# Kernel tuning notes

Hardware: AMD Instinct MI355X
Metric: run time of the kernel (lower is better)

The kernel has to match this reference:

```python
import jax, jax.numpy as jnp
import numpy as np

D_IN = 1024
D_OUT = 1024
N = 4096


def setup_inputs() -> dict:
    key = jax.random.key(0)
    kx, kq, kk, kv = jax.random.split(key, 4)
    x = jax.random.normal(kx, (N, D_IN), dtype=jnp.float32)
    # weights stored as [d_in, d_out] so that x @ W == torch Linear(x)
    s = 1.0 / np.sqrt(D_IN)
    W_q = jax.random.uniform(kq, (D_IN, D_OUT), jnp.float32, -s, s)
    W_k = jax.random.uniform(kk, (D_IN, D_OUT), jnp.float32, -s, s)
    W_v = jax.random.uniform(kv, (D_IN, D_OUT), jnp.float32, -s, s)
    return {"x": x, "W_q": W_q, "W_k": W_k, "W_v": W_v}


def reference(x, W_q, W_k, W_v):
    # x: [N, d_in]; projections -> [N, d_out]
    q = x @ W_q
    k = x @ W_k
    v = x @ W_v
    scale = 1.0 / jnp.sqrt(jnp.asarray(k.shape[-1], dtype=q.dtype))
    scores = (q @ k.T) * scale            # [N, N]
    weights = jax.nn.softmax(scores, axis=-1)
    return weights @ v                     # [N, d_out]
```

## Files before the change

### kernel.cpp

```cpp
#include <hip/hip_runtime.h>
#include <math.h>

typedef _Float16 f16;
typedef __attribute__((ext_vector_type(8))) _Float16 f16x8;
typedef __attribute__((ext_vector_type(4))) _Float16 f16x4;
typedef __attribute__((ext_vector_type(4))) float f32x4;

#define NSEQ 4096
#define DIN 1024
#define DOUT 1024

__device__ __forceinline__ void load16(const void* g, void* l) {
    __builtin_amdgcn_global_load_lds(
        (const __attribute__((address_space(1))) unsigned int*)g,
        (__attribute__((address_space(3))) unsigned int*)l, 16, 0, 0);
}

template <typename OutT>
__global__ __launch_bounds__(256, 2)
void gemm_bt(const f16* __restrict__ A, const f16* __restrict__ B,
             OutT* __restrict__ C, int M, int N, int K,
             int lda, int ldb, int ldc, float scale,
             long bStrideZ, long cStrideZ)
{
    B += (long)blockIdx.z * bStrideZ;
    C += (long)blockIdx.z * cStrideZ;
    __shared__ f16 As[2 * 128 * 32];
    __shared__ f16 Bs[2 * 128 * 32];

    int gx = gridDim.x;
    int bid = blockIdx.y * gx + blockIdx.x;
    int xcd = bid & 7, s = bid >> 3;
    int px = s & 7, rest = s >> 3;
    int py = rest & 3, chunk = rest >> 2;
    int pg = xcd + (chunk << 3);
    int pcols = gx >> 3;
    int lp = 31 - __clz(pcols);
    int bx = ((pg & (pcols - 1)) << 3) + px;
    int by = ((pg >> lp) << 2) + py;

    const int t    = threadIdx.x;
    const int lane = t & 63;
    const int wave = t >> 6;
    const int wm   = (wave >> 1) * 64;
    const int wn   = (wave & 1) * 64;
    const int tile_m = by * 128;
    const int tile_n = bx * 128;
    const int quad = lane >> 4;
    const int l16  = lane & 15;
    const int srow = t >> 2;
    const int scol = (t & 3) * 8;

    f32x4 acc[4][4];
#pragma unroll
    for (int i = 0; i < 4; i++)
#pragma unroll
        for (int j = 0; j < 4; j++)
            acc[i][j] = (f32x4){0.f, 0.f, 0.f, 0.f};

    const f16* Ab = A + (long)(tile_m + srow) * lda + scol;
    const f16* Bb = B + (long)(tile_n + srow) * ldb + scol;
    f16* Asd = As + t * 8;
    f16* Bsd = Bs + t * 8;

    for (int k0 = 0; k0 < K; k0 += 64) {
        load16(Ab + k0, Asd);
        load16(Ab + (long)64 * lda + k0, Asd + 2048);
        load16(Ab + k0 + 32, Asd + 4096);
        load16(Ab + (long)64 * lda + k0 + 32, Asd + 4096 + 2048);
        load16(Bb + k0, Bsd);
        load16(Bb + (long)64 * ldb + k0, Bsd + 2048);
        load16(Bb + k0 + 32, Bsd + 4096);
        load16(Bb + (long)64 * ldb + k0 + 32, Bsd + 4096 + 2048);
        __syncthreads();
#pragma unroll
        for (int p = 0; p < 2; p++) {
            f16x8 a[4], b[4];
#pragma unroll
            for (int i = 0; i < 4; i++)
                a[i] = *(const f16x8*)(As + p * 4096 + (wm + i * 16 + l16) * 32 + quad * 8);
#pragma unroll
            for (int j = 0; j < 4; j++)
                b[j] = *(const f16x8*)(Bs + p * 4096 + (wn + j * 16 + l16) * 32 + quad * 8);
#pragma unroll
            for (int i = 0; i < 4; i++)
#pragma unroll
                for (int j = 0; j < 4; j++)
                    acc[i][j] = __builtin_amdgcn_mfma_f32_16x16x32_f16(
                        a[i], b[j], acc[i][j], 0, 0, 0);
        }
        __syncthreads();
    }
#pragma unroll
    for (int i = 0; i < 4; i++)
#pragma unroll
        for (int j = 0; j < 4; j++)
#pragma unroll
            for (int r = 0; r < 4; r++) {
                int row = tile_m + wm + i * 16 + quad * 4 + r;
                int col = tile_n + wn + j * 16 + l16;
                C[(long)row * ldc + col] = (OutT)(acc[i][j][r] * scale);
            }
}

__global__ void cvt_f16(const float* __restrict__ x, f16* __restrict__ y) {
    int i = (blockIdx.x * 256 + threadIdx.x) * 4;
    f32x4 v = *(const f32x4*)(x + i);
    f16x4 o;
    o.x = (f16)v.x; o.y = (f16)v.y; o.z = (f16)v.z; o.w = (f16)v.w;
    *(f16x4*)(y + i) = o;
}

__global__ void transpose_w3(const float* __restrict__ W0, const float* __restrict__ W1,
                             const float* __restrict__ W2, f16* __restrict__ Wt) {
    __shared__ f16 tile[64][65];
    const float* W = blockIdx.z == 0 ? W0 : (blockIdx.z == 1 ? W1 : W2);
    f16* O = Wt + (long)blockIdx.z * DIN * DOUT;
    int r0 = blockIdx.y * 64;
    int c0 = blockIdx.x * 64;
    int tx = threadIdx.x & 63, ty = threadIdx.x >> 6;
#pragma unroll
    for (int i = 0; i < 16; i++)
        tile[ty + i * 4][tx] = (f16)W[(long)(r0 + ty + i * 4) * DOUT + c0 + tx];
    __syncthreads();
#pragma unroll
    for (int i = 0; i < 16; i++)
        O[(long)(c0 + ty + i * 4) * DIN + r0 + tx] = tile[tx][ty + i * 4];
}

__global__ void transpose_v(const f16* __restrict__ V, f16* __restrict__ Vt) {
    __shared__ f16 tile[64][65];
    int r0 = blockIdx.y * 64;
    int c0 = blockIdx.x * 64;
    int tx = threadIdx.x & 63, ty = threadIdx.x >> 6;
#pragma unroll
    for (int i = 0; i < 16; i++)
        tile[ty + i * 4][tx] = V[(long)(r0 + ty + i * 4) * DOUT + c0 + tx];
    __syncthreads();
#pragma unroll
    for (int i = 0; i < 16; i++)
        Vt[(long)(c0 + ty + i * 4) * NSEQ + r0 + tx] = tile[tx][ty + i * 4];
}

__global__ __launch_bounds__(256)
void softmax_f16(f16* __restrict__ S) {
    const int t = threadIdx.x;
    f16* row = S + (long)blockIdx.x * NSEQ;
    float v[16];
    f16x8 x0 = *(const f16x8*)(row + t * 8);
    f16x8 x1 = *(const f16x8*)(row + 2048 + t * 8);
#pragma unroll
    for (int i = 0; i < 8; i++) { v[i] = (float)x0[i]; v[8 + i] = (float)x1[i]; }
    int lane = t & 63, wave = t >> 6;
    float m = -1e30f;
#pragma unroll
    for (int i = 0; i < 16; i++) m = fmaxf(m, v[i]);
#pragma unroll
    for (int off = 32; off; off >>= 1) m = fmaxf(m, __shfl_xor(m, off, 64));
    __shared__ float redm[4];
    if (lane == 0) redm[wave] = m;
    __syncthreads();
    m = fmaxf(fmaxf(redm[0], redm[1]), fmaxf(redm[2], redm[3]));
    float sum = 0.f;
#pragma unroll
    for (int i = 0; i < 16; i++) { v[i] = __expf(v[i] - m); sum += v[i]; }
#pragma unroll
    for (int off = 32; off; off >>= 1) sum += __shfl_xor(sum, off, 64);
    __shared__ float reds[4];
    if (lane == 0) reds[wave] = sum;
    __syncthreads();
    sum = reds[0] + reds[1] + reds[2] + reds[3];
    float inv = 1.f / sum;
    f16x8 o0, o1;
#pragma unroll
    for (int i = 0; i < 8; i++) {
        o0[i] = (f16)(v[i] * inv);
        o1[i] = (f16)(v[8 + i] * inv);
    }
    *(f16x8*)(row + t * 8) = o0;
    *(f16x8*)(row + 2048 + t * 8) = o1;
}

extern "C" void kernel_launch(void* const* d_in, const int* in_sizes, int n_in,
                              void* d_out, int out_size, void* d_ws, size_t ws_size,
                              hipStream_t stream) {
    const float* x  = (const float*)d_in[0];
    const float* Wq = (const float*)d_in[1];
    const float* Wk = (const float*)d_in[2];
    const float* Wv = (const float*)d_in[3];
    float* out = (float*)d_out;
    char* ws = (char*)d_ws;
    const size_t MB = 1ull << 20;
    f16* xb = (f16*)(ws);
    f16* Wt = (f16*)(ws + 8 * MB);
    f16* Qb = (f16*)(ws + 14 * MB);
    f16* Kb = (f16*)(ws + 22 * MB);
    f16* Vb = (f16*)(ws + 30 * MB);
    f16* Vt = (f16*)(ws);
    f16* S  = (f16*)(ws + 38 * MB);

    cvt_f16<<<4096, 256, 0, stream>>>(x, xb);
    transpose_w3<<<dim3(16, 16, 3), 256, 0, stream>>>(Wq, Wk, Wv, Wt);
    gemm_bt<f16><<<dim3(8, 32, 3), 256, 0, stream>>>(
        xb, Wt, Qb, NSEQ, DOUT, DIN, DIN, DIN, DOUT, 1.0f,
        (long)DIN * DOUT, (long)NSEQ * DOUT);
    transpose_v<<<dim3(16, 64), 256, 0, stream>>>(Vb, Vt);
    gemm_bt<f16><<<dim3(32, 32, 1), 256, 0, stream>>>(
        Qb, Kb, S, NSEQ, NSEQ, DOUT, DOUT, DOUT, NSEQ, 0.03125f, 0, 0);
    softmax_f16<<<4096, 256, 0, stream>>>(S);
    gemm_bt<float><<<dim3(8, 32, 1), 256, 0, stream>>>(
        S, Vt, out, NSEQ, DOUT, NSEQ, NSEQ, NSEQ, DOUT, 1.0f, 0, 0);
}
```

Before: 236.1 us.

## Split-K final GEMM, fuse V transpose into projection, swizzle LDS, merge prep kernels

The final S@V GEMM is split four ways along K across blockIdx.z, writing fp32 partials that a new reduce kernel sums. This gives 1024 blocks instead of 256 and fills the GPU better. The V projection now writes its output transposed straight from the epilogue, which removes the separate transpose_v kernel. An XOR swizzle on LDS column placement targets bank conflicts, and the x conversion and weight transpose are merged into one launch. The cost is extra fp32 partial traffic plus a reduce pass.

```diff
diff --git a/kernel.cpp b/kernel.cpp
--- a/kernel.cpp
+++ b/kernel.cpp
@@ -19,12 +19,16 @@
 template <typename OutT>
 __global__ __launch_bounds__(256, 2)
 void gemm_bt(const f16* __restrict__ A, const f16* __restrict__ B,
-             OutT* __restrict__ C, int M, int N, int K,
-             int lda, int ldb, int ldc, float scale,
-             long bStrideZ, long cStrideZ)
+             OutT* __restrict__ c0, OutT* __restrict__ c1,
+             OutT* __restrict__ c2, OutT* __restrict__ c3,
+             int M, int N, int K, int lda, int ldb, int ldc, float scale,
+             long aStrideZ, long bStrideZ,
+             f16* __restrict__ TC, int tz, int ldt)
 {
-    B += (long)blockIdx.z * bStrideZ;
-    C += (long)blockIdx.z * cStrideZ;
+    const int z = blockIdx.z;
+    A += (long)z * aStrideZ;
+    B += (long)z * bStrideZ;
+    OutT* C = z == 0 ? c0 : (z == 1 ? c1 : (z == 2 ? c2 : c3));
     __shared__ f16 As[2 * 128 * 32];
     __shared__ f16 Bs[2 * 128 * 32];
 
@@ -49,7 +53,8 @@
     const int quad = lane >> 4;
     const int l16  = lane & 15;
     const int srow = t >> 2;
-    const int scol = (t & 3) * 8;
+    const int scol = ((t & 3) ^ (srow & 3)) * 8;
+    const int qx8 = (quad ^ (l16 & 3)) * 8;
 
     f32x4 acc[4][4];
 #pragma unroll
@@ -78,10 +83,10 @@
             f16x8 a[4], b[4];
 #pragma unroll
             for (int i = 0; i < 4; i++)
-                a[i] = *(const f16x8*)(As + p * 4096 + (wm + i * 16 + l16) * 32 + quad * 8);
+                a[i] = *(const f16x8*)(As + p * 4096 + (wm + i * 16 + l16) * 32 + qx8);
 #pragma unroll
             for (int j = 0; j < 4; j++)
-                b[j] = *(const f16x8*)(Bs + p * 4096 + (wn + j * 16 + l16) * 32 + quad * 8);
+                b[j] = *(const f16x8*)(Bs + p * 4096 + (wn + j * 16 + l16) * 32 + qx8);
 #pragma unroll
             for (int i = 0; i < 4; i++)
 #pragma unroll
@@ -91,28 +96,48 @@
         }
         __syncthreads();
     }
-#pragma unroll
-    for (int i = 0; i < 4; i++)
-#pragma unroll
-        for (int j = 0; j < 4; j++)
-#pragma unroll
-            for (int r = 0; r < 4; r++) {
-                int row = tile_m + wm + i * 16 + quad * 4 + r;
-                int col = tile_n + wn + j * 16 + l16;
-                C[(long)row * ldc + col] = (OutT)(acc[i][j][r] * scale);
+    if (TC != nullptr && z == tz) {
+#pragma unroll
+        for (int i = 0; i < 4; i++)
+#pragma unroll
+            for (int j = 0; j < 4; j++) {
+                f16x4 o;
+#pragma unroll
+                for (int r = 0; r < 4; r++) o[r] = (f16)(acc[i][j][r] * scale);
+                int row0 = tile_m + wm + i * 16 + quad * 4;
+                int col  = tile_n + wn + j * 16 + l16;
+                *(f16x4*)(TC + (long)col * ldt + row0) = o;
             }
-}
-
-__global__ void cvt_f16(const float* __restrict__ x, f16* __restrict__ y) {
-    int i = (blockIdx.x * 256 + threadIdx.x) * 4;
-    f32x4 v = *(const f32x4*)(x + i);
-    f16x4 o;
-    o.x = (f16)v.x; o.y = (f16)v.y; o.z = (f16)v.z; o.w = (f16)v.w;
-    *(f16x4*)(y + i) = o;
-}
-
-__global__ void transpose_w3(const float* __restrict__ W0, const float* __restrict__ W1,
-                             const float* __restrict__ W2, f16* __restrict__ Wt) {
+    } else {
+#pragma unroll
+        for (int i = 0; i < 4; i++)
+#pragma unroll
+            for (int j = 0; j < 4; j++)
+#pragma unroll
+                for (int r = 0; r < 4; r++) {
+                    int row = tile_m + wm + i * 16 + quad * 4 + r;
+                    int col = tile_n + wn + j * 16 + l16;
+                    C[(long)row * ldc + col] = (OutT)(acc[i][j][r] * scale);
+                }
+    }
+}
+
+__global__ void prep(const float* __restrict__ x,
+                     const float* __restrict__ W0, const float* __restrict__ W1,
+                     const float* __restrict__ W2,
+                     f16* __restrict__ xb, f16* __restrict__ Wt) {
+    if (blockIdx.z == 3) {
+        long base = ((long)(blockIdx.y * 16 + blockIdx.x) * 256 + threadIdx.x) * 4;
+#pragma unroll
+        for (int it = 0; it < 16; it++) {
+            long i = base + (long)it * (256 * 256 * 4);
+            f32x4 v = *(const f32x4*)(x + i);
+            f16x4 o;
+            o.x = (f16)v.x; o.y = (f16)v.y; o.z = (f16)v.z; o.w = (f16)v.w;
+            *(f16x4*)(xb + i) = o;
+        }
+        return;
+    }
     __shared__ f16 tile[64][65];
     const float* W = blockIdx.z == 0 ? W0 : (blockIdx.z == 1 ? W1 : W2);
     f16* O = Wt + (long)blockIdx.z * DIN * DOUT;
@@ -128,18 +153,14 @@
         O[(long)(c0 + ty + i * 4) * DIN + r0 + tx] = tile[tx][ty + i * 4];
 }
 
-__global__ void transpose_v(const f16* __restrict__ V, f16* __restrict__ Vt) {
-    __shared__ f16 tile[64][65];
-    int r0 = blockIdx.y * 64;
-    int c0 = blockIdx.x * 64;
-    int tx = threadIdx.x & 63, ty = threadIdx.x >> 6;
-#pragma unroll
-    for (int i = 0; i < 16; i++)
-        tile[ty + i * 4][tx] = V[(long)(r0 + ty + i * 4) * DOUT + c0 + tx];
-    __syncthreads();
-#pragma unroll
-    for (int i = 0; i < 16; i++)
-        Vt[(long)(c0 + ty + i * 4) * NSEQ + r0 + tx] = tile[tx][ty + i * 4];
+__global__ void reduce_add4(const float* __restrict__ p0, const float* __restrict__ p1,
+                            const float* __restrict__ p2, float* __restrict__ out) {
+    int i = (blockIdx.x * 256 + threadIdx.x) * 4;
+    f32x4 a = *(const f32x4*)(p0 + i);
+    f32x4 b = *(const f32x4*)(p1 + i);
+    f32x4 c = *(const f32x4*)(p2 + i);
+    f32x4 d = *(const f32x4*)(out + i);
+    *(f32x4*)(out + i) = (a + b) + (c + d);
 }
 
 __global__ __launch_bounds__(256)
@@ -191,23 +212,26 @@
     float* out = (float*)d_out;
     char* ws = (char*)d_ws;
     const size_t MB = 1ull << 20;
-    f16* xb = (f16*)(ws);
-    f16* Wt = (f16*)(ws + 8 * MB);
-    f16* Qb = (f16*)(ws + 14 * MB);
-    f16* Kb = (f16*)(ws + 22 * MB);
-    f16* Vb = (f16*)(ws + 30 * MB);
-    f16* Vt = (f16*)(ws);
-    f16* S  = (f16*)(ws + 38 * MB);
-
-    cvt_f16<<<4096, 256, 0, stream>>>(x, xb);
-    transpose_w3<<<dim3(16, 16, 3), 256, 0, stream>>>(Wq, Wk, Wv, Wt);
+    f16* xb  = (f16*)(ws);
+    f16* Wt  = (f16*)(ws + 8 * MB);
+    f16* Qb  = (f16*)(ws + 14 * MB);
+    f16* Kb  = (f16*)(ws + 22 * MB);
+    f16* Vt  = (f16*)(ws + 30 * MB);
+    f16* S   = (f16*)(ws + 38 * MB);
+    float* Pp0 = (float*)(ws + 70 * MB);
+    float* Pp1 = (float*)(ws + 86 * MB);
+    float* Pp2 = (float*)(ws + 14 * MB);
+
+    prep<<<dim3(16, 16, 4), 256, 0, stream>>>(x, Wq, Wk, Wv, xb, Wt);
     gemm_bt<f16><<<dim3(8, 32, 3), 256, 0, stream>>>(
-        xb, Wt, Qb, NSEQ, DOUT, DIN, DIN, DIN, DOUT, 1.0f,
-        (long)DIN * DOUT, (long)NSEQ * DOUT);
-    transpose_v<<<dim3(16, 64), 256, 0, stream>>>(Vb, Vt);
+        xb, Wt, Qb, Kb, Qb, Qb, NSEQ, DOUT, DIN, DIN, DIN, DOUT, 1.0f,
+        0, (long)DIN * DOUT, Vt, 2, NSEQ);
     gemm_bt<f16><<<dim3(32, 32, 1), 256, 0, stream>>>(
-        Qb, Kb, S, NSEQ, NSEQ, DOUT, DOUT, DOUT, NSEQ, 0.03125f, 0, 0);
+        Qb, Kb, S, S, S, S, NSEQ, NSEQ, DOUT, DOUT, DOUT, NSEQ, 0.03125f,
+        0, 0, nullptr, -1, 0);
     softmax_f16<<<4096, 256, 0, stream>>>(S);
-    gemm_bt<float><<<dim3(8, 32, 1), 256, 0, stream>>>(
-        S, Vt, out, NSEQ, DOUT, NSEQ, NSEQ, NSEQ, DOUT, 1.0f, 0, 0);
-}
+    gemm_bt<float><<<dim3(8, 32, 4), 256, 0, stream>>>(
+        S, Vt, Pp0, Pp1, Pp2, out, NSEQ, DOUT, 1024, NSEQ, NSEQ, DOUT, 1.0f,
+        1024, 1024, nullptr, -1, 0);
+    reduce_add4<<<4096, 256, 0, stream>>>(Pp0, Pp1, Pp2, out);
+}
```

Measured after the change: 214.9 us. 1.1x faster.
